# Optimization experiments

Measured on AMD Instinct MI355X. Metric: run time of the kernel, lower is better.

Reference implementation:

```python
import jax, jax.numpy as jnp
import numpy as np

N_NODES = 100000
K_HOPS = 2


def _add_self_loops(edge_index, n):
    loop = jnp.arange(n, dtype=edge_index.dtype)
    src = jnp.concatenate([edge_index[0], loop])
    dst = jnp.concatenate([edge_index[1], loop])
    return src, dst


def _gcn_norm(src, dst, n):
    # symmetric normalization D^-1/2 (A+I) D^-1/2
    deg = jax.ops.segment_sum(jnp.ones_like(dst, dtype=jnp.float32), dst, num_segments=n)
    dinv = jnp.where(deg > 0, jax.lax.rsqrt(deg), 0.0)
    return dinv[src] * dinv[dst]  # [E]


def setup_inputs() -> dict:
    key = jax.random.key(0)
    k1, k2, k3, k4, k5 = jax.random.split(key, 5)
    in_f, out_f = 128, 64
    x = jax.random.normal(k1, (N_NODES, in_f), dtype=jnp.float32)
    edge_index = jax.random.randint(k2, (2, 1600000), 0, N_NODES, dtype=jnp.int64)
    s1 = 1.0 / np.sqrt(in_f)
    W1 = jax.random.uniform(k3, (in_f, in_f), dtype=jnp.float32, minval=-s1, maxval=s1)
    b1 = jnp.zeros((in_f,), dtype=jnp.float32)
    W2 = jax.random.uniform(k4, (out_f, in_f), dtype=jnp.float32, minval=-s1, maxval=s1)
    b2 = jnp.zeros((out_f,), dtype=jnp.float32)
    return {"x": x, "edge_index": edge_index, "W1": W1, "b1": b1, "W2": W2, "b2": b2}


def reference(x, edge_index, W1, b1, W2, b2):
    n = x.shape[0]
    src, dst = _add_self_loops(edge_index, n)
    norm = _gcn_norm(src, dst, n)
    for _ in range(K_HOPS):
        msg = x[src] * norm[:, None]                      # [E+N, F] gather
        x = jax.ops.segment_sum(msg, dst, num_segments=n)  # scatter-add
    # transform: Linear -> ReLU -> Linear -> log_softmax
    h = jax.nn.relu(x @ W1.T + b1)
    logits = h @ W2.T + b2
    return jax.nn.log_softmax(logits, axis=1)
```

## Files before the change

kernel.cpp:

```cpp
#include <hip/hip_runtime.h>
#include <math.h>

#define CAP 64
#define NSLICE 256
#define SLMAX 392

typedef __attribute__((ext_vector_type(8))) short short8;
typedef __attribute__((ext_vector_type(4))) float f32x4;
typedef __attribute__((ext_vector_type(4))) int int4v;

static __device__ inline unsigned short f2bf(float f) {
    unsigned int u = __float_as_uint(f);
    u += 0x7fffu + ((u >> 16) & 1u);
    return (unsigned short)(u >> 16);
}
static __device__ inline float bf_lo(unsigned int u) { return __uint_as_float(u << 16); }
static __device__ inline float bf_hi(unsigned int u) { return __uint_as_float(u & 0xffff0000u); }
static __device__ inline unsigned int pack2(float lo, float hi) {
    return ((unsigned int)f2bf(hi) << 16) | (unsigned int)f2bf(lo);
}


__global__ __launch_bounds__(256) void part_k(
    const int* __restrict__ dst, const int* __restrict__ src, int E,
    unsigned long long mul, int slice_sz, int qcap,
    unsigned int* __restrict__ queue, int* __restrict__ qcnt, int gb_p,
    const float2* __restrict__ W1f, unsigned int* __restrict__ w1b, int n1,
    const float2* __restrict__ W2f, unsigned int* __restrict__ w2b, int n2)
{
    if (blockIdx.x >= gb_p) {
        int i = (blockIdx.x - gb_p) * 256 + threadIdx.x;
        if (i < n1) {
            float2 v = W1f[i];
            w1b[i] = pack2(v.x, v.y);
        } else if (i < n1 + n2) {
            float2 v = W2f[i - n1];
            w2b[i - n1] = pack2(v.x, v.y);
        }
        return;
    }

    __shared__ int lcnt[NSLICE];
    __shared__ int gbase[NSLICE];
    lcnt[threadIdx.x] = 0;
    __syncthreads();

    int base = blockIdx.x * 2048 + threadIdx.x * 8;
    int nv = E - base; nv = nv > 8 ? 8 : (nv < 0 ? 0 : nv);

    int d[8], sv[8], sl[8], lp[8];
    if (nv == 8) {
        int4v da = __builtin_nontemporal_load((const int4v*)(dst + base));
        int4v db = __builtin_nontemporal_load((const int4v*)(dst + base + 4));
        int4v sa = __builtin_nontemporal_load((const int4v*)(src + base));
        int4v sb = __builtin_nontemporal_load((const int4v*)(src + base + 4));
#pragma unroll
        for (int j = 0; j < 4; j++) {
            d[j] = da[j]; sv[j] = sa[j];
            d[4 + j] = db[j]; sv[4 + j] = sb[j];
        }
    } else {
        for (int j = 0; j < nv; j++) { d[j] = dst[base + j]; sv[j] = src[base + j]; }
    }

#pragma unroll
    for (int j = 0; j < 8; j++) {
        if (j < nv) {
            sl[j] = (int)(((unsigned long long)(unsigned)d[j] * mul) >> 40);
            lp[j] = atomicAdd(&lcnt[sl[j]], 1);
        }
    }
    __syncthreads();
    gbase[threadIdx.x] = atomicAdd(&qcnt[threadIdx.x], lcnt[threadIdx.x]);
    __syncthreads();
#pragma unroll
    for (int j = 0; j < 8; j++) {
        if (j < nv) {
            int p = gbase[sl[j]] + lp[j];
            unsigned int dloc = (unsigned int)(d[j] - sl[j] * slice_sz);
            if (p < qcap) queue[(size_t)sl[j] * qcap + p] = (dloc << 20) | (unsigned int)sv[j];
        }
    }
}


__global__ __launch_bounds__(256) void scat_lds_k(
    const unsigned int* __restrict__ queue, const int* __restrict__ qcnt, int qcap,
    int sl, int n, const float4* __restrict__ x4,
    int* __restrict__ cnt, float* __restrict__ dinv,
    int* __restrict__ bkt, unsigned int* __restrict__ xb)
{
    int s  = blockIdx.x;
    int lo = s * sl;
    int hi = lo + sl < n ? lo + sl : n;
    int nn = hi - lo;
    if (nn <= 0) return;

    __shared__ int cur[SLMAX];
    __shared__ float sdv[SLMAX];
    for (int i = threadIdx.x; i < nn; i += 256) cur[i] = 0;
    __syncthreads();

    int m = qcnt[s]; if (m > qcap) m = qcap;
    const unsigned int* __restrict__ q = queue + (size_t)s * qcap;
    for (int i = threadIdx.x; i < m; i += 256) {
        unsigned int r = __builtin_nontemporal_load(q + i);
        int sv   = (int)(r & 0xFFFFFu);
        int dloc = (int)(r >> 20);
        int pos = atomicAdd(&cur[dloc], 1);
        if (pos < CAP) bkt[(size_t)(lo + dloc) * CAP + pos] = sv;
    }
    __syncthreads();
    for (int i = threadIdx.x; i < nn; i += 256) {
        int c = cur[i];
        cnt[lo + i] = c;
        float dv = rsqrtf((float)(c + 1));
        dinv[lo + i] = dv;
        sdv[i] = dv;
    }
    __syncthreads();
    for (int j = threadIdx.x; j < nn * 32; j += 256) {
        int nl = j >> 5, f4 = j & 31;
        float4 v = x4[(size_t)(lo + nl) * 32 + f4];
        float sc = sdv[nl];
        uint2 o;
        o.x = pack2(v.x * sc, v.y * sc);
        o.y = pack2(v.z * sc, v.w * sc);
        ((uint2*)xb)[(size_t)(lo + nl) * 32 + f4] = o;
    }
}


template<bool SQ>
__global__ __launch_bounds__(256) void gather_b_k(
    const unsigned int* __restrict__ xin,
    const int* __restrict__ cnt, const int* __restrict__ bkt,
    const float* __restrict__ dinv,
    unsigned int* __restrict__ xout, int n)
{
    int v = blockIdx.x * 4 + (threadIdx.x >> 6);
    if (v >= n) return;
    int l = threadIdx.x & 63;
    int c = cnt[v]; if (c > CAP) c = CAP;
    c = __builtin_amdgcn_readfirstlane(c);

    int be = bkt[(size_t)v * CAP + l];
    unsigned int us = xin[(size_t)v * 64 + l];
    float ax = 0.f, ay = 0.f;

    int i = 0;
    for (; i + 16 <= c; i += 16) {
        unsigned int u[16];
#pragma unroll
        for (int j = 0; j < 16; j++) {
            int s = __builtin_amdgcn_readlane(be, i + j);
            u[j] = xin[(size_t)s * 64 + l];
        }
#pragma unroll
        for (int j = 0; j < 16; j++) { ax += bf_lo(u[j]); ay += bf_hi(u[j]); }
    }
    for (; i + 8 <= c; i += 8) {
        unsigned int u[8];
#pragma unroll
        for (int j = 0; j < 8; j++) {
            int s = __builtin_amdgcn_readlane(be, i + j);
            u[j] = xin[(size_t)s * 64 + l];
        }
#pragma unroll
        for (int j = 0; j < 8; j++) { ax += bf_lo(u[j]); ay += bf_hi(u[j]); }
    }
    for (; i + 4 <= c; i += 4) {
        unsigned int u[4];
#pragma unroll
        for (int j = 0; j < 4; j++) {
            int s = __builtin_amdgcn_readlane(be, i + j);
            u[j] = xin[(size_t)s * 64 + l];
        }
#pragma unroll
        for (int j = 0; j < 4; j++) { ax += bf_lo(u[j]); ay += bf_hi(u[j]); }
    }
    for (; i < c; i++) {
        int s = __builtin_amdgcn_readlane(be, i);
        unsigned int u = xin[(size_t)s * 64 + l];
        ax += bf_lo(u); ay += bf_hi(u);
    }

    ax += bf_lo(us);
    ay += bf_hi(us);

    float dv = dinv[v];
    float sc = SQ ? dv * dv : dv;
    xout[(size_t)v * 64 + l] = pack2(ax * sc, ay * sc);
}

__global__ __launch_bounds__(256) void transform_mfma_k(
    const unsigned short* __restrict__ x2b,
    const unsigned short* __restrict__ w1b,
    const float* __restrict__ b1,
    const unsigned short* __restrict__ w2b,
    const float* __restrict__ b2,
    float* __restrict__ out, int n)
{
    __shared__ __align__(16) unsigned short Hs[64][152];

    int t = threadIdx.x;
    int w = t >> 6;
    int l = t & 63;
    int lg = l >> 4;
    int ll = l & 15;
    int node0 = blockIdx.x * 64;

    int nrow = node0 + w * 16 + ll;
    int crow = nrow < n ? nrow : (n - 1);
    const unsigned short* xrow = x2b + (size_t)crow * 128 + lg * 8;
    short8 a[4];
#pragma unroll
    for (int kb = 0; kb < 4; kb++)
        a[kb] = *(const short8*)(xrow + kb * 32);

    f32x4 acc[8];
#pragma unroll
    for (int nt = 0; nt < 8; nt++) {
        float bv = b1[nt * 16 + ll];
        acc[nt][0] = bv; acc[nt][1] = bv; acc[nt][2] = bv; acc[nt][3] = bv;
    }
#pragma unroll
    for (int nt = 0; nt < 8; nt++) {
        const unsigned short* wrow = w1b + (size_t)(nt * 16 + ll) * 128 + lg * 8;
#pragma unroll
        for (int kb = 0; kb < 4; kb++) {
            short8 bf = *(const short8*)(wrow + kb * 32);
            acc[nt] = __builtin_amdgcn_mfma_f32_16x16x32_bf16(a[kb], bf, acc[nt], 0, 0, 0);
        }
    }

#pragma unroll
    for (int nt = 0; nt < 8; nt++) {
#pragma unroll
        for (int r = 0; r < 4; r++) {
            float hv = fmaxf(acc[nt][r], 0.f);
            Hs[w * 16 + lg * 4 + r][nt * 16 + ll] = f2bf(hv);
        }
    }

    short8 ha[4];
#pragma unroll
    for (int kb = 0; kb < 4; kb++)
        ha[kb] = *(const short8*)&Hs[w * 16 + ll][kb * 32 + lg * 8];

    f32x4 acc2[4];
#pragma unroll
    for (int nt = 0; nt < 4; nt++) {
        float bv = b2[nt * 16 + ll];
        acc2[nt][0] = bv; acc2[nt][1] = bv; acc2[nt][2] = bv; acc2[nt][3] = bv;
        const unsigned short* wrow = w2b + (size_t)(nt * 16 + ll) * 128 + lg * 8;
#pragma unroll
        for (int kb = 0; kb < 4; kb++) {
            short8 bf = *(const short8*)(wrow + kb * 32);
            acc2[nt] = __builtin_amdgcn_mfma_f32_16x16x32_bf16(ha[kb], bf, acc2[nt], 0, 0, 0);
        }
    }

#pragma unroll
    for (int r = 0; r < 4; r++) {
        float m = fmaxf(fmaxf(acc2[0][r], acc2[1][r]), fmaxf(acc2[2][r], acc2[3][r]));
        m = fmaxf(m, __shfl_xor(m, 1));
        m = fmaxf(m, __shfl_xor(m, 2));
        m = fmaxf(m, __shfl_xor(m, 4));
        m = fmaxf(m, __shfl_xor(m, 8));
        float s = __expf(acc2[0][r] - m) + __expf(acc2[1][r] - m) +
                  __expf(acc2[2][r] - m) + __expf(acc2[3][r] - m);
        s += __shfl_xor(s, 1);
        s += __shfl_xor(s, 2);
        s += __shfl_xor(s, 4);
        s += __shfl_xor(s, 8);
        float lse = m + __logf(s);
        int node = node0 + w * 16 + lg * 4 + r;
        if (node < n) {
#pragma unroll
            for (int nt = 0; nt < 4; nt++)
                out[(size_t)node * 64 + nt * 16 + ll] = acc2[nt][r] - lse;
        }
    }
}


static inline size_t align256(size_t x) { return (x + 255) & ~(size_t)255; }

extern "C" void kernel_launch(void* const* d_in, const int* in_sizes, int n_in,
                              void* d_out, int out_size, void* d_ws, size_t ws_size,
                              hipStream_t stream) {
    const float* x  = (const float*)d_in[0];
    const int*   ei = (const int*)d_in[1];
    const float* W1 = (const float*)d_in[2];
    const float* b1 = (const float*)d_in[3];
    const float* W2 = (const float*)d_in[4];
    const float* b2 = (const float*)d_in[5];
    float* out = (float*)d_out;

    int n = in_sizes[0] / 128;
    int E = in_sizes[1] / 2;
    const int* src = ei;
    const int* dst = ei + E;

    int sl = (n + NSLICE - 1) / NSLICE;
    int qcap = sl * 64;
    unsigned long long mul = ((1ULL << 40) + (unsigned long long)sl - 1) / (unsigned long long)sl;

    char* w = (char*)d_ws;
    size_t off = 0;
    int*          cnt  = (int*)(w + off);          off += align256((size_t)n * sizeof(int));
    int*          qcnt = (int*)(w + off);          off += align256(NSLICE * sizeof(int));
    float*        dinv = (float*)(w + off);        off += align256((size_t)n * sizeof(float));
    int*          bkt  = (int*)(w + off);          off += align256((size_t)n * CAP * sizeof(int));
    size_t xb_bytes = (size_t)NSLICE * qcap * 4;
    unsigned int* xb   = (unsigned int*)(w + off); off += align256(xb_bytes);
    unsigned int* z1b  = (unsigned int*)(w + off); off += align256((size_t)n * 64 * sizeof(unsigned int));
    unsigned int* x2b  = (unsigned int*)(w + off); off += align256((size_t)n * 64 * sizeof(unsigned int));
    unsigned int* w1b  = (unsigned int*)(w + off); off += align256((size_t)128 * 64 * sizeof(unsigned int));
    unsigned int* w2b  = (unsigned int*)(w + off);
    unsigned int* queue = xb;

    int tb = 256;
    int gb_g = (n + 3) / 4;
    int gb_p = (E + 2047) / 2048;
    int n1 = 128 * 128 / 2, n2 = 64 * 128 / 2;
    int gb_w = (n1 + n2 + tb - 1) / tb;

    (void)hipMemsetAsync(qcnt, 0, NSLICE * sizeof(int), stream);
    part_k<<<gb_p + gb_w, tb, 0, stream>>>(dst, src, E, mul, sl, qcap, queue, qcnt,
                                           gb_p, (const float2*)W1, w1b, n1,
                                           (const float2*)W2, w2b, n2);
    scat_lds_k<<<NSLICE, tb, 0, stream>>>(queue, qcnt, qcap, sl, n, (const float4*)x,
                                          cnt, dinv, bkt, xb);
    gather_b_k<true ><<<gb_g, tb, 0, stream>>>(xb,  cnt, bkt, dinv, z1b, n);
    gather_b_k<false><<<gb_g, tb, 0, stream>>>(z1b, cnt, bkt, dinv, x2b, n);
    transform_mfma_k<<<(n + 63) / 64, tb, 0, stream>>>(
        (const unsigned short*)x2b, (const unsigned short*)w1b, b1,
        (const unsigned short*)w2b, b2, out, n);
}
```

Baseline: 226.8 us.

## Split neighbor gather across feature halves with two edges per wavefront

Rewrites the bf16 neighbor-gather kernel so each block handles one 64-feature half of four nodes, and each wavefront processes two edges concurrently in its two 32-lane halves, merging partial sums with a cross-half shuffle. The grid is doubled and the cascaded unrolled loops are replaced by a single predicated 8-edge loop using shuffles for neighbor indices. The aim is more memory-level parallelism and occupancy for the latency-bound gather, at the cost of reading bucket lists twice and issuing narrower 128-byte row loads.

```diff
diff --git a/kernel.cpp b/kernel.cpp
--- a/kernel.cpp
+++ b/kernel.cpp
@@ -132,65 +132,53 @@
 
 
 template<bool SQ>
-__global__ __launch_bounds__(256) void gather_b_k(
+__global__ __launch_bounds__(256) void gather_h_k(
     const unsigned int* __restrict__ xin,
     const int* __restrict__ cnt, const int* __restrict__ bkt,
     const float* __restrict__ dinv,
     unsigned int* __restrict__ xout, int n)
 {
-    int v = blockIdx.x * 4 + (threadIdx.x >> 6);
+    int b = blockIdx.x;
+    int h = b & 1;
+    int v = (b >> 1) * 4 + (threadIdx.x >> 6);
     if (v >= n) return;
     int l = threadIdx.x & 63;
+    int g = l >> 5;
+    int lh = l & 31;
     int c = cnt[v]; if (c > CAP) c = CAP;
     c = __builtin_amdgcn_readfirstlane(c);
 
     int be = bkt[(size_t)v * CAP + l];
-    unsigned int us = xin[(size_t)v * 64 + l];
+    const unsigned int* __restrict__ xh = xin + h * 32;
+    unsigned int us = xh[(size_t)v * 64 + lh];
     float ax = 0.f, ay = 0.f;
 
-    int i = 0;
-    for (; i + 16 <= c; i += 16) {
-        unsigned int u[16];
-#pragma unroll
-        for (int j = 0; j < 16; j++) {
-            int s = __builtin_amdgcn_readlane(be, i + j);
-            u[j] = xin[(size_t)s * 64 + l];
-        }
-#pragma unroll
-        for (int j = 0; j < 16; j++) { ax += bf_lo(u[j]); ay += bf_hi(u[j]); }
-    }
-    for (; i + 8 <= c; i += 8) {
-        unsigned int u[8];
-#pragma unroll
-        for (int j = 0; j < 8; j++) {
-            int s = __builtin_amdgcn_readlane(be, i + j);
-            u[j] = xin[(size_t)s * 64 + l];
-        }
-#pragma unroll
-        for (int j = 0; j < 8; j++) { ax += bf_lo(u[j]); ay += bf_hi(u[j]); }
-    }
-    for (; i + 4 <= c; i += 4) {
+    for (int i = 0; i < c; i += 8) {
         unsigned int u[4];
-#pragma unroll
-        for (int j = 0; j < 4; j++) {
-            int s = __builtin_amdgcn_readlane(be, i + j);
-            u[j] = xin[(size_t)s * 64 + l];
-        }
-#pragma unroll
-        for (int j = 0; j < 4; j++) { ax += bf_lo(u[j]); ay += bf_hi(u[j]); }
-    }
-    for (; i < c; i++) {
-        int s = __builtin_amdgcn_readlane(be, i);
-        unsigned int u = xin[(size_t)s * 64 + l];
-        ax += bf_lo(u); ay += bf_hi(u);
-    }
-
+        int act[4];
+#pragma unroll
+        for (int k = 0; k < 4; k++) {
+            int e = i + 2 * k + g;
+            act[k] = e < c;
+            int ec = act[k] ? e : (c - 1);
+            int s = __shfl(be, ec);
+            u[k] = xh[(size_t)s * 64 + lh];
+        }
+#pragma unroll
+        for (int k = 0; k < 4; k++) {
+            if (act[k]) { ax += bf_lo(u[k]); ay += bf_hi(u[k]); }
+        }
+    }
+
+    ax += __shfl_xor(ax, 32);
+    ay += __shfl_xor(ay, 32);
     ax += bf_lo(us);
     ay += bf_hi(us);
 
     float dv = dinv[v];
     float sc = SQ ? dv * dv : dv;
-    xout[(size_t)v * 64 + l] = pack2(ax * sc, ay * sc);
+    unsigned int o = pack2(ax * sc, ay * sc);
+    if (l < 32) xout[(size_t)v * 64 + h * 32 + l] = o;
 }
 
 __global__ __launch_bounds__(256) void transform_mfma_k(
@@ -322,7 +310,7 @@
     unsigned int* queue = xb;
 
     int tb = 256;
-    int gb_g = (n + 3) / 4;
+    int gb_g = 2 * ((n + 3) / 4);
     int gb_p = (E + 2047) / 2048;
     int n1 = 128 * 128 / 2, n2 = 64 * 128 / 2;
     int gb_w = (n1 + n2 + tb - 1) / tb;
@@ -333,8 +321,8 @@
                                            (const float2*)W2, w2b, n2);
     scat_lds_k<<<NSLICE, tb, 0, stream>>>(queue, qcnt, qcap, sl, n, (const float4*)x,
                                           cnt, dinv, bkt, xb);
-    gather_b_k<true ><<<gb_g, tb, 0, stream>>>(xb,  cnt, bkt, dinv, z1b, n);
-    gather_b_k<false><<<gb_g, tb, 0, stream>>>(z1b, cnt, bkt, dinv, x2b, n);
+    gather_h_k<true ><<<gb_g, tb, 0, stream>>>(xb,  cnt, bkt, dinv, z1b, n);
+    gather_h_k<false><<<gb_g, tb, 0, stream>>>(z1b, cnt, bkt, dinv, x2b, n);
     transform_mfma_k<<<(n + 63) / 64, tb, 0, stream>>>(
         (const unsigned short*)x2b, (const unsigned short*)w1b, b1,
         (const unsigned short*)w2b, b2, out, n);
```

Result: slower. 273.5 us (+20.6%).
